# Optimization experiments

Hardware: AMD Instinct MI355X
Metric: run time of the kernel (lower is better)

Reference implementation:

```python
import jax, jax.numpy as jnp
import numpy as np

N_NODES = 100000
N_EDGES = 1600000
D_IN = 128
D_OUT = 128


def setup_inputs() -> dict:
    key = jax.random.key(0)
    k1, k2, k3 = jax.random.split(key, 3)
    x = jax.random.normal(k1, (N_NODES, D_IN), dtype=jnp.float32)
    edge_index = jax.random.randint(k2, (2, N_EDGES), 0, N_NODES, dtype=jnp.int64)
    # glorot-style init for the lazily-created weight
    scale = jnp.sqrt(6.0 / (D_IN + D_OUT)).astype(jnp.float32)
    weight = jax.random.uniform(k3, (D_IN, D_OUT), dtype=jnp.float32, minval=-1.0, maxval=1.0) * scale
    bias = jnp.zeros((D_OUT,), dtype=jnp.float32)
    return {"x": x, "edge_index": edge_index, "weight": weight, "bias": bias}


def reference(x, edge_index, weight, bias):
    N = x.shape[0]
    row, col = edge_index[0], edge_index[1]
    # add_remaining_self_loops: drop existing self-loops (equivalently zero their
    # weight) and append a self-loop of weight 1.0 for every node (improved=False).
    ew = jnp.where(row == col, 0.0, 1.0).astype(x.dtype)
    loop = jnp.arange(N, dtype=row.dtype)
    row = jnp.concatenate([row, loop])
    col = jnp.concatenate([col, loop])
    ew = jnp.concatenate([ew, jnp.ones((N,), dtype=x.dtype)])
    # degree via scatter-add on destination (col), deg^{-1/2} with inf -> 0
    deg = jax.ops.segment_sum(ew, col, num_segments=N)
    deg_inv_sqrt = jnp.where(deg > 0, jax.lax.rsqrt(deg), 0.0).astype(x.dtype)
    norm = deg_inv_sqrt[row] * ew * deg_inv_sqrt[col]  # [E+N]
    # dense transform then gather-scale-scatter (GCN message passing, aggr='add')
    xw = x @ weight  # [N, D_OUT]
    msgs = norm[:, None] * xw[row]  # [E+N, D_OUT] gather on source nodes
    out = jax.ops.segment_sum(msgs, col, num_segments=N)  # scatter-add to dest
    return out + bias
```

## Files before the change

### kernel.cpp

```cpp
#include <hip/hip_runtime.h>
#include <hip/hip_bf16.h>

#define NN 100000
#define NE 1600000
#define D  128
#define NPAD 100352
#define NBLK 782
#define CAP  64

#define BSH    9
#define NB_C   196
#define CAPB   9216
#define PCHUNK 8192
#define PEPT   8
#define NPART  196

typedef __attribute__((ext_vector_type(8))) short short8;
typedef __attribute__((ext_vector_type(4))) float floatx4;
typedef __attribute__((ext_vector_type(4))) unsigned int uintx4;

__device__ __forceinline__ unsigned short f2b(float f) {
    __hip_bfloat16 h = __float2bfloat16(f);
    return *(unsigned short*)&h;
}

__device__ __forceinline__ void acc8(float (&a)[8], uintx4 v) {
    a[0] += __uint_as_float(v.x << 16);
    a[1] += __uint_as_float(v.x & 0xFFFF0000u);
    a[2] += __uint_as_float(v.y << 16);
    a[3] += __uint_as_float(v.y & 0xFFFF0000u);
    a[4] += __uint_as_float(v.z << 16);
    a[5] += __uint_as_float(v.z & 0xFFFF0000u);
    a[6] += __uint_as_float(v.w << 16);
    a[7] += __uint_as_float(v.w & 0xFFFF0000u);
}

__device__ __forceinline__ int swz(int row, int col_us) {
    return row * 128 + (col_us ^ ((row & 7) << 3));
}

__global__ __launch_bounds__(1024) void k_part(const int* __restrict__ row,
                                               const int* __restrict__ col,
                                               int* __restrict__ bcnt,
                                               unsigned int* __restrict__ edgesP) {
    __shared__ int cur[NB_C], basep[NB_C];
    int t = threadIdx.x;
    size_t e0 = (size_t)blockIdx.x * PCHUNK;

    for (int i = t; i < NB_C; i += 1024) cur[i] = 0;
    __syncthreads();

    unsigned int val[PEPT];
    int bk[PEPT], rk[PEPT];
#pragma unroll
    for (int i = 0; i < PEPT; ++i) {
        size_t e = e0 + i * 1024 + t;
        bk[i] = -1;
        if (e < NE) {
            int r = row[e], c = col[e];
            if (r != c) {
                bk[i]  = c >> BSH;
                val[i] = (unsigned)r | ((unsigned)(c & 511) << 17);
                rk[i]  = atomicAdd(&cur[bk[i]], 1);
            }
        }
    }
    __syncthreads();

    for (int i = t; i < NB_C; i += 1024)
        basep[i] = cur[i] ? atomicAdd(&bcnt[i], cur[i]) : 0;
    __syncthreads();

#pragma unroll
    for (int i = 0; i < PEPT; ++i) {
        if (bk[i] >= 0) {
            int pos = basep[bk[i]] + rk[i];
            if (pos < CAPB) edgesP[(size_t)bk[i] * CAPB + pos] = val[i];
        }
    }
}

__global__ __launch_bounds__(1024) void k_fine(const int* __restrict__ bcnt,
                                               const unsigned int* __restrict__ edgesP,
                                               int* __restrict__ counts,
                                               float* __restrict__ dinv,
                                               int* __restrict__ srcs) {
    __shared__ int cnt[512];
    int t = threadIdx.x, b = blockIdx.x;
    int n0 = b << BSH;
    for (int i = t; i < 512; i += 1024) cnt[i] = 0;
    __syncthreads();

    int m = min(bcnt[b], CAPB);
    const unsigned int* ep = edgesP + (size_t)b * CAPB;
    for (int i = t; i < m; i += 1024) {
        unsigned int v = ep[i];
        int c0 = v >> 17;
        int s  = v & 0x1FFFF;
        int pos = atomicAdd(&cnt[c0], 1);
        if (pos < CAP) srcs[(size_t)(n0 + c0) * CAP + pos] = s;
    }
    __syncthreads();
    for (int i = t; i < 512; i += 1024) {
        int n = n0 + i;
        int cv = cnt[i];
        counts[n] = min(cv, CAP);
        dinv[n] = rsqrtf((float)cv + 1.0f);
    }
}

__global__ __launch_bounds__(256, 2) void k_gemm_mfma(const float* __restrict__ x,
                                                      const float* __restrict__ w,
                                                      const float* __restrict__ dinv,
                                                      unsigned short* __restrict__ yw) {
    __shared__ unsigned short sX[128 * 128];
    __shared__ unsigned short sW[128 * 128];
    __shared__ float sD[128];
    int tid = threadIdx.x;
    long row0 = (long)blockIdx.x * 128;

    if (tid < 128) {
        long gr = row0 + tid;
        sD[tid] = (gr < NN) ? dinv[gr] : 0.0f;
    }
#pragma unroll
    for (int j = 0; j < 16; ++j) {
        int i4 = tid + j * 256;
        int i = i4 * 4;
        int k = i >> 7, n = i & 127;
        floatx4 v = *(const floatx4*)(w + i);
        sW[swz(n + 0, k)] = f2b(v.x);
        sW[swz(n + 1, k)] = f2b(v.y);
        sW[swz(n + 2, k)] = f2b(v.z);
        sW[swz(n + 3, k)] = f2b(v.w);
    }
#pragma unroll
    for (int j = 0; j < 16; ++j) {
        int i = tid + j * 256;
        int r = i >> 5, q = i & 31;
        floatx4 v = {0.f, 0.f, 0.f, 0.f};
        long gr = row0 + r;
        if (gr < NN) v = __builtin_nontemporal_load((const floatx4*)(x + gr * D + q * 4));
        ushort4 u;
        u.x = f2b(v.x); u.y = f2b(v.y); u.z = f2b(v.z); u.w = f2b(v.w);
        *(ushort4*)&sX[swz(r, q * 4)] = u;
    }
    __syncthreads();

    int lane = tid & 63, wave = tid >> 6;
    int wm = (wave & 1) * 64, wn = (wave >> 1) * 64;
    int lrow = lane & 15, lkb = (lane >> 4) * 8;

    floatx4 acc[4][4] = {};
#pragma unroll
    for (int kc = 0; kc < 4; ++kc) {
        int kb = kc * 32 + lkb;
        short8 bfr[4];
#pragma unroll
        for (int tn = 0; tn < 4; ++tn)
            bfr[tn] = *(const short8*)&sW[swz(wn + tn * 16 + lrow, kb)];
#pragma unroll
        for (int tm = 0; tm < 4; ++tm) {
            short8 afr = *(const short8*)&sX[swz(wm + tm * 16 + lrow, kb)];
#pragma unroll
            for (int tn = 0; tn < 4; ++tn)
                acc[tm][tn] = __builtin_amdgcn_mfma_f32_16x16x32_bf16(afr, bfr[tn], acc[tm][tn], 0, 0, 0);
        }
    }

    __syncthreads();

    int orow = (lane >> 4) * 4;
    int ocol = lane & 15;
#pragma unroll
    for (int tm = 0; tm < 4; ++tm) {
#pragma unroll
        for (int reg = 0; reg < 4; ++reg) {
            int rt = wm + tm * 16 + orow + reg;
            float dm = sD[rt];
#pragma unroll
            for (int tn = 0; tn < 4; ++tn)
                sX[swz(rt, wn + tn * 16 + ocol)] = f2b(acc[tm][tn][reg] * dm);
        }
    }
    __syncthreads();

#pragma unroll
    for (int j = 0; j < 8; ++j) {
        int i = tid + j * 256;
        int r = i >> 4, cg = i & 15;
        long gr = row0 + r;
        if (gr < NN) {
            uint4 v = *(const uint4*)&sX[swz(r, cg * 8)];
            *(uint4*)(yw + gr * D + cg * 8) = v;
        }
    }
}

__global__ __launch_bounds__(256) void k_agg(const int* __restrict__ counts,
                                             const int* __restrict__ srcs,
                                             const float* __restrict__ dinv,
                                             const uintx4* __restrict__ yw4,
                                             const float* __restrict__ bias,
                                             float* __restrict__ out) {
    int lane = threadIdx.x & 63;
    int c = blockIdx.x * 4 + (threadIdx.x >> 6);
    int g = lane >> 4, f = lane & 15;

    int cnt0 = min(counts[c], 63);
    const int* sp = srcs + (size_t)c * CAP;
    int mysrc = c;
    if (lane >= 1 && lane <= cnt0) mysrc = __builtin_nontemporal_load(sp + lane - 1);
    int ec = cnt0 + 1;

    float dc = dinv[c];

    float a[8] = {0.f, 0.f, 0.f, 0.f, 0.f, 0.f, 0.f, 0.f};

    int p = 0;
    for (; p + 16 <= ec; p += 16) {
        uintx4 v[4];
#pragma unroll
        for (int i = 0; i < 4; ++i) {
            int s = __shfl(mysrc, p + i * 4 + g);
            v[i] = yw4[(size_t)s * 16 + f];
        }
#pragma unroll
        for (int i = 0; i < 4; ++i) acc8(a, v[i]);
    }
    if (p + 8 <= ec) {
        uintx4 v[2];
#pragma unroll
        for (int i = 0; i < 2; ++i) {
            int s = __shfl(mysrc, p + i * 4 + g);
            v[i] = yw4[(size_t)s * 16 + f];
        }
#pragma unroll
        for (int i = 0; i < 2; ++i) acc8(a, v[i]);
        p += 8;
    }
    if (p + 4 <= ec) {
        int s = __shfl(mysrc, p + g);
        uintx4 v = yw4[(size_t)s * 16 + f];
        acc8(a, v);
        p += 4;
    }
    int r = ec - p;
    if (r > 0) {
        int s = __shfl(mysrc, p + ((g < r) ? g : 0));
        uintx4 v = yw4[(size_t)s * 16 + f];
        if (g < r) acc8(a, v);
    }

#pragma unroll
    for (int j = 0; j < 8; ++j) a[j] += __shfl_xor(a[j], 16);
#pragma unroll
    for (int j = 0; j < 8; ++j) a[j] += __shfl_xor(a[j], 32);

    if (g == 0) {
        const floatx4* b4 = (const floatx4*)bias;
        floatx4 b0 = b4[f * 2], b1 = b4[f * 2 + 1];
        floatx4 o0, o1;
        o0.x = dc * a[0] + b0.x;  o0.y = dc * a[1] + b0.y;
        o0.z = dc * a[2] + b0.z;  o0.w = dc * a[3] + b0.w;
        o1.x = dc * a[4] + b1.x;  o1.y = dc * a[5] + b1.y;
        o1.z = dc * a[6] + b1.z;  o1.w = dc * a[7] + b1.w;
        floatx4* op = (floatx4*)(out + (size_t)c * D + f * 8);
        __builtin_nontemporal_store(o0, op);
        __builtin_nontemporal_store(o1, op + 1);
    }
}

extern "C" void kernel_launch(void* const* d_in, const int* in_sizes, int n_in,
                              void* d_out, int out_size, void* d_ws, size_t ws_size,
                              hipStream_t stream) {
    const float* x    = (const float*)d_in[0];
    const int*   ei   = (const int*)d_in[1];
    const float* w    = (const float*)d_in[2];
    const float* bias = (const float*)d_in[3];
    float*       out  = (float*)d_out;

    const int* row = ei;
    const int* col = ei + NE;

    int*   counts = (int*)d_ws;
    float* dinv   = (float*)(counts + NPAD);
    int*   srcs   = (int*)(dinv + NPAD);
    unsigned short* yw = (unsigned short*)(srcs + (size_t)NN * CAP);
    int*   bcnt   = (int*)(yw + (size_t)NN * D);
    unsigned int* edgesP = (unsigned int*)yw;

    hipMemsetAsync(bcnt, 0, NB_C * sizeof(int), stream);

    k_part<<<NPART, 1024, 0, stream>>>(row, col, bcnt, edgesP);
    k_fine<<<NB_C, 1024, 0, stream>>>(bcnt, edgesP, counts, dinv, srcs);
    k_gemm_mfma<<<NBLK, 256, 0, stream>>>(x, w, dinv, yw);
    k_agg<<<NN / 4, 256, 0, stream>>>(counts, srcs, dinv, (const uintx4*)yw, bias, out);
}
```

Baseline: 223.1 us.

## Fuse edge partitioning with GEMM in one launch and move source scaling into aggregation

Merges the edge-partition kernel and the dense X@W MFMA kernel into one launch that interleaves partition blocks and GEMM blocks, so the two independent stages can overlap on the GPU. The GEMM no longer depends on dinv, so the source-side normalization moves into the aggregation kernel as a per-edge dinv multiply, broadcast via shuffles. The partition scratch buffer is relocated to the output buffer so it no longer aliases yw. The aggregation loop gains an extra per-edge dinv gather and multiply. Partition blocks are also made smaller.

```diff
diff --git a/kernel.cpp b/kernel.cpp
--- a/kernel.cpp
+++ b/kernel.cpp
@@ -11,9 +11,10 @@
 #define BSH    9
 #define NB_C   196
 #define CAPB   9216
-#define PCHUNK 8192
+#define PCHUNK 2048
 #define PEPT   8
-#define NPART  196
+#define NPART  782
+#define FUSED_BLOCKS (NPART + NBLK)
 
 typedef __attribute__((ext_vector_type(8))) short short8;
 typedef __attribute__((ext_vector_type(4))) float floatx4;
@@ -24,58 +25,142 @@
     return *(unsigned short*)&h;
 }
 
-__device__ __forceinline__ void acc8(float (&a)[8], uintx4 v) {
-    a[0] += __uint_as_float(v.x << 16);
-    a[1] += __uint_as_float(v.x & 0xFFFF0000u);
-    a[2] += __uint_as_float(v.y << 16);
-    a[3] += __uint_as_float(v.y & 0xFFFF0000u);
-    a[4] += __uint_as_float(v.z << 16);
-    a[5] += __uint_as_float(v.z & 0xFFFF0000u);
-    a[6] += __uint_as_float(v.w << 16);
-    a[7] += __uint_as_float(v.w & 0xFFFF0000u);
+__device__ __forceinline__ void acc8f(float (&a)[8], uintx4 v, float d) {
+    a[0] += d * __uint_as_float(v.x << 16);
+    a[1] += d * __uint_as_float(v.x & 0xFFFF0000u);
+    a[2] += d * __uint_as_float(v.y << 16);
+    a[3] += d * __uint_as_float(v.y & 0xFFFF0000u);
+    a[4] += d * __uint_as_float(v.z << 16);
+    a[5] += d * __uint_as_float(v.z & 0xFFFF0000u);
+    a[6] += d * __uint_as_float(v.w << 16);
+    a[7] += d * __uint_as_float(v.w & 0xFFFF0000u);
 }
 
 __device__ __forceinline__ int swz(int row, int col_us) {
     return row * 128 + (col_us ^ ((row & 7) << 3));
 }
 
-__global__ __launch_bounds__(1024) void k_part(const int* __restrict__ row,
-                                               const int* __restrict__ col,
-                                               int* __restrict__ bcnt,
-                                               unsigned int* __restrict__ edgesP) {
-    __shared__ int cur[NB_C], basep[NB_C];
-    int t = threadIdx.x;
-    size_t e0 = (size_t)blockIdx.x * PCHUNK;
-
-    for (int i = t; i < NB_C; i += 1024) cur[i] = 0;
-    __syncthreads();
-
-    unsigned int val[PEPT];
-    int bk[PEPT], rk[PEPT];
-#pragma unroll
-    for (int i = 0; i < PEPT; ++i) {
-        size_t e = e0 + i * 1024 + t;
-        bk[i] = -1;
-        if (e < NE) {
-            int r = row[e], c = col[e];
-            if (r != c) {
-                bk[i]  = c >> BSH;
-                val[i] = (unsigned)r | ((unsigned)(c & 511) << 17);
-                rk[i]  = atomicAdd(&cur[bk[i]], 1);
-            }
-        }
-    }
-    __syncthreads();
-
-    for (int i = t; i < NB_C; i += 1024)
-        basep[i] = cur[i] ? atomicAdd(&bcnt[i], cur[i]) : 0;
-    __syncthreads();
-
-#pragma unroll
-    for (int i = 0; i < PEPT; ++i) {
-        if (bk[i] >= 0) {
-            int pos = basep[bk[i]] + rk[i];
-            if (pos < CAPB) edgesP[(size_t)bk[i] * CAPB + pos] = val[i];
+__global__ __launch_bounds__(256, 2) void k_fused(const float* __restrict__ x,
+                                                  const float* __restrict__ w,
+                                                  const int* __restrict__ row,
+                                                  const int* __restrict__ col,
+                                                  int* __restrict__ bcnt,
+                                                  unsigned int* __restrict__ edgesP,
+                                                  unsigned short* __restrict__ yw) {
+    __shared__ __align__(16) unsigned short smem[2 * 128 * 128];
+    int tid = threadIdx.x;
+    int pid = blockIdx.x >> 1;
+
+    if ((blockIdx.x & 1) == 0) {
+        int* cur   = (int*)smem;
+        int* basep = cur + NB_C;
+        size_t e0 = (size_t)pid * PCHUNK;
+
+        for (int i = tid; i < NB_C; i += 256) cur[i] = 0;
+        __syncthreads();
+
+        unsigned int val[PEPT];
+        int bk[PEPT], rk[PEPT];
+#pragma unroll
+        for (int i = 0; i < PEPT; ++i) {
+            size_t e = e0 + i * 256 + tid;
+            bk[i] = -1;
+            if (e < NE) {
+                int r = row[e], c = col[e];
+                if (r != c) {
+                    bk[i]  = c >> BSH;
+                    val[i] = (unsigned)r | ((unsigned)(c & 511) << 17);
+                    rk[i]  = atomicAdd(&cur[bk[i]], 1);
+                }
+            }
+        }
+        __syncthreads();
+
+        for (int i = tid; i < NB_C; i += 256)
+            basep[i] = cur[i] ? atomicAdd(&bcnt[i], cur[i]) : 0;
+        __syncthreads();
+
+#pragma unroll
+        for (int i = 0; i < PEPT; ++i) {
+            if (bk[i] >= 0) {
+                int pos = basep[bk[i]] + rk[i];
+                if (pos < CAPB) edgesP[(size_t)bk[i] * CAPB + pos] = val[i];
+            }
+        }
+    } else {
+        unsigned short* sX = smem;
+        unsigned short* sW = smem + 128 * 128;
+        long row0 = (long)pid * 128;
+
+#pragma unroll
+        for (int j = 0; j < 16; ++j) {
+            int i4 = tid + j * 256;
+            int i = i4 * 4;
+            int k = i >> 7, n = i & 127;
+            floatx4 v = *(const floatx4*)(w + i);
+            sW[swz(n + 0, k)] = f2b(v.x);
+            sW[swz(n + 1, k)] = f2b(v.y);
+            sW[swz(n + 2, k)] = f2b(v.z);
+            sW[swz(n + 3, k)] = f2b(v.w);
+        }
+#pragma unroll
+        for (int j = 0; j < 16; ++j) {
+            int i = tid + j * 256;
+            int r = i >> 5, q = i & 31;
+            floatx4 v = {0.f, 0.f, 0.f, 0.f};
+            long gr = row0 + r;
+            if (gr < NN) v = __builtin_nontemporal_load((const floatx4*)(x + gr * D + q * 4));
+            ushort4 u;
+            u.x = f2b(v.x); u.y = f2b(v.y); u.z = f2b(v.z); u.w = f2b(v.w);
+            *(ushort4*)&sX[swz(r, q * 4)] = u;
+        }
+        __syncthreads();
+
+        int lane = tid & 63, wave = tid >> 6;
+        int wm = (wave & 1) * 64, wn = (wave >> 1) * 64;
+        int lrow = lane & 15, lkb = (lane >> 4) * 8;
+
+        floatx4 acc[4][4] = {};
+#pragma unroll
+        for (int kc = 0; kc < 4; ++kc) {
+            int kb = kc * 32 + lkb;
+            short8 bfr[4];
+#pragma unroll
+            for (int tn = 0; tn < 4; ++tn)
+                bfr[tn] = *(const short8*)&sW[swz(wn + tn * 16 + lrow, kb)];
+#pragma unroll
+            for (int tm = 0; tm < 4; ++tm) {
+                short8 afr = *(const short8*)&sX[swz(wm + tm * 16 + lrow, kb)];
+#pragma unroll
+                for (int tn = 0; tn < 4; ++tn)
+                    acc[tm][tn] = __builtin_amdgcn_mfma_f32_16x16x32_bf16(afr, bfr[tn], acc[tm][tn], 0, 0, 0);
+            }
+        }
+
+        __syncthreads();
+        int orow = (lane >> 4) * 4;
+        int ocol = lane & 15;
+#pragma unroll
+        for (int tm = 0; tm < 4; ++tm) {
+#pragma unroll
+            for (int reg = 0; reg < 4; ++reg) {
+                int rt = wm + tm * 16 + orow + reg;
+#pragma unroll
+                for (int tn = 0; tn < 4; ++tn)
+                    sX[swz(rt, wn + tn * 16 + ocol)] = f2b(acc[tm][tn][reg]);
+            }
+        }
+        __syncthreads();
+
+#pragma unroll
+        for (int j = 0; j < 8; ++j) {
+            int i = tid + j * 256;
+            int r = i >> 4, cg = i & 15;
+            long gr = row0 + r;
+            if (gr < NN) {
+                uint4 v = *(const uint4*)&sX[swz(r, cg * 8)];
+                *(uint4*)(yw + gr * D + cg * 8) = v;
+            }
         }
     }
 }
@@ -109,94 +194,6 @@
     }
 }
 
-__global__ __launch_bounds__(256, 2) void k_gemm_mfma(const float* __restrict__ x,
-                                                      const float* __restrict__ w,
-                                                      const float* __restrict__ dinv,
-                                                      unsigned short* __restrict__ yw) {
-    __shared__ unsigned short sX[128 * 128];
-    __shared__ unsigned short sW[128 * 128];
-    __shared__ float sD[128];
-    int tid = threadIdx.x;
-    long row0 = (long)blockIdx.x * 128;
-
-    if (tid < 128) {
-        long gr = row0 + tid;
-        sD[tid] = (gr < NN) ? dinv[gr] : 0.0f;
-    }
-#pragma unroll
-    for (int j = 0; j < 16; ++j) {
-        int i4 = tid + j * 256;
-        int i = i4 * 4;
-        int k = i >> 7, n = i & 127;
-        floatx4 v = *(const floatx4*)(w + i);
-        sW[swz(n + 0, k)] = f2b(v.x);
-        sW[swz(n + 1, k)] = f2b(v.y);
-        sW[swz(n + 2, k)] = f2b(v.z);
-        sW[swz(n + 3, k)] = f2b(v.w);
-    }
-#pragma unroll
-    for (int j = 0; j < 16; ++j) {
-        int i = tid + j * 256;
-        int r = i >> 5, q = i & 31;
-        floatx4 v = {0.f, 0.f, 0.f, 0.f};
-        long gr = row0 + r;
-        if (gr < NN) v = __builtin_nontemporal_load((const floatx4*)(x + gr * D + q * 4));
-        ushort4 u;
-        u.x = f2b(v.x); u.y = f2b(v.y); u.z = f2b(v.z); u.w = f2b(v.w);
-        *(ushort4*)&sX[swz(r, q * 4)] = u;
-    }
-    __syncthreads();
-
-    int lane = tid & 63, wave = tid >> 6;
-    int wm = (wave & 1) * 64, wn = (wave >> 1) * 64;
-    int lrow = lane & 15, lkb = (lane >> 4) * 8;
-
-    floatx4 acc[4][4] = {};
-#pragma unroll
-    for (int kc = 0; kc < 4; ++kc) {
-        int kb = kc * 32 + lkb;
-        short8 bfr[4];
-#pragma unroll
-        for (int tn = 0; tn < 4; ++tn)
-            bfr[tn] = *(const short8*)&sW[swz(wn + tn * 16 + lrow, kb)];
-#pragma unroll
-        for (int tm = 0; tm < 4; ++tm) {
-            short8 afr = *(const short8*)&sX[swz(wm + tm * 16 + lrow, kb)];
-#pragma unroll
-            for (int tn = 0; tn < 4; ++tn)
-                acc[tm][tn] = __builtin_amdgcn_mfma_f32_16x16x32_bf16(afr, bfr[tn], acc[tm][tn], 0, 0, 0);
-        }
-    }
-
-    __syncthreads();
-
-    int orow = (lane >> 4) * 4;
-    int ocol = lane & 15;
-#pragma unroll
-    for (int tm = 0; tm < 4; ++tm) {
-#pragma unroll
-        for (int reg = 0; reg < 4; ++reg) {
-            int rt = wm + tm * 16 + orow + reg;
-            float dm = sD[rt];
-#pragma unroll
-            for (int tn = 0; tn < 4; ++tn)
-                sX[swz(rt, wn + tn * 16 + ocol)] = f2b(acc[tm][tn][reg] * dm);
-        }
-    }
-    __syncthreads();
-
-#pragma unroll
-    for (int j = 0; j < 8; ++j) {
-        int i = tid + j * 256;
-        int r = i >> 4, cg = i & 15;
-        long gr = row0 + r;
-        if (gr < NN) {
-            uint4 v = *(const uint4*)&sX[swz(r, cg * 8)];
-            *(uint4*)(yw + gr * D + cg * 8) = v;
-        }
-    }
-}
-
 __global__ __launch_bounds__(256) void k_agg(const int* __restrict__ counts,
                                              const int* __restrict__ srcs,
                                              const float* __restrict__ dinv,
@@ -211,6 +208,7 @@
     const int* sp = srcs + (size_t)c * CAP;
     int mysrc = c;
     if (lane >= 1 && lane <= cnt0) mysrc = __builtin_nontemporal_load(sp + lane - 1);
+    float myds = dinv[mysrc];
     int ec = cnt0 + 1;
 
     float dc = dinv[c];
@@ -219,37 +217,44 @@
 
     int p = 0;
     for (; p + 16 <= ec; p += 16) {
-        uintx4 v[4];
+        uintx4 v[4]; float d[4];
 #pragma unroll
         for (int i = 0; i < 4; ++i) {
-            int s = __shfl(mysrc, p + i * 4 + g);
+            int ix = p + i * 4 + g;
+            int s = __shfl(mysrc, ix);
+            d[i] = __shfl(myds, ix);
             v[i] = yw4[(size_t)s * 16 + f];
         }
 #pragma unroll
-        for (int i = 0; i < 4; ++i) acc8(a, v[i]);
+        for (int i = 0; i < 4; ++i) acc8f(a, v[i], d[i]);
     }
     if (p + 8 <= ec) {
-        uintx4 v[2];
+        uintx4 v[2]; float d[2];
 #pragma unroll
         for (int i = 0; i < 2; ++i) {
-            int s = __shfl(mysrc, p + i * 4 + g);
+            int ix = p + i * 4 + g;
+            int s = __shfl(mysrc, ix);
+            d[i] = __shfl(myds, ix);
             v[i] = yw4[(size_t)s * 16 + f];
         }
 #pragma unroll
-        for (int i = 0; i < 2; ++i) acc8(a, v[i]);
+        for (int i = 0; i < 2; ++i) acc8f(a, v[i], d[i]);
         p += 8;
     }
     if (p + 4 <= ec) {
         int s = __shfl(mysrc, p + g);
+        float d = __shfl(myds, p + g);
         uintx4 v = yw4[(size_t)s * 16 + f];
-        acc8(a, v);
+        acc8f(a, v, d);
         p += 4;
     }
     int r = ec - p;
     if (r > 0) {
-        int s = __shfl(mysrc, p + ((g < r) ? g : 0));
+        int ix = p + ((g < r) ? g : 0);
+        int s = __shfl(mysrc, ix);
+        float d = __shfl(myds, ix);
         uintx4 v = yw4[(size_t)s * 16 + f];
-        if (g < r) acc8(a, v);
+        if (g < r) acc8f(a, v, d);
     }
 
 #pragma unroll
@@ -288,12 +293,11 @@
     int*   srcs   = (int*)(dinv + NPAD);
     unsigned short* yw = (unsigned short*)(srcs + (size_t)NN * CAP);
     int*   bcnt   = (int*)(yw + (size_t)NN * D);
-    unsigned int* edgesP = (unsigned int*)yw;
+    unsigned int* edgesP = (unsigned int*)d_out;
 
     hipMemsetAsync(bcnt, 0, NB_C * sizeof(int), stream);
 
-    k_part<<<NPART, 1024, 0, stream>>>(row, col, bcnt, edgesP);
+    k_fused<<<FUSED_BLOCKS, 256, 0, stream>>>(x, w, row, col, bcnt, edgesP, yw);
     k_fine<<<NB_C, 1024, 0, stream>>>(bcnt, edgesP, counts, dinv, srcs);
-    k_gemm_mfma<<<NBLK, 256, 0, stream>>>(x, w, dinv, yw);
     k_agg<<<NN / 4, 256, 0, stream>>>(counts, srcs, dinv, (const uintx4*)yw, bias, out);
 }
```

Result: slower. 235.6 us (+5.6%).
